# Kernel tuning notes

Hardware: AMD Instinct MI355X
Metric: run time of the kernel (lower is better)

The kernel has to match this reference:

```python
import jax, jax.numpy as jnp
import numpy as np
from jax import lax

NUM_HEADS = 8
DIM = 192
EPS = 1e-12  # torch F.normalize eps


def setup_inputs() -> dict:
    key = jax.random.key(0)
    k1, k2, k3, k4 = jax.random.split(key, 4)
    b, c, h, w = 8, DIM, 128, 128
    x = jax.random.normal(k1, (b, c, h, w), dtype=jnp.float32)
    # 1x1 qkv conv weight stored as [3c, c]; depthwise 3x3 weight [3c,1,3,3]; proj 1x1 [c,c]
    w_qkv = jax.random.normal(k2, (3 * c, c), dtype=jnp.float32) * (1.0 / np.sqrt(c))
    w_dw = jax.random.normal(k3, (3 * c, 1, 3, 3), dtype=jnp.float32) * (1.0 / 3.0)
    w_proj = jax.random.normal(k4, (c, c), dtype=jnp.float32) * (1.0 / np.sqrt(c))
    temperature = jnp.ones((NUM_HEADS, 1, 1), dtype=jnp.float32)
    return {"x": x, "w_qkv": w_qkv, "w_dw": w_dw, "w_proj": w_proj, "temperature": temperature}


def _l2_normalize(t):
    # matches torch.nn.functional.normalize(dim=-1, eps=1e-12)
    n = jnp.sqrt(jnp.sum(t * t, axis=-1, keepdims=True))
    return t / jnp.maximum(n, EPS)


def reference(x, w_qkv, w_dw, w_proj, temperature):
    b, c, h, w = x.shape
    heads = NUM_HEADS
    cd = c // heads  # per-head channel dim
    # 1x1 qkv conv (no bias) as einsum
    qkv = jnp.einsum('bchw,oc->bohw', x, w_qkv)  # [b, 3c, h, w]
    # depthwise 3x3 conv, groups = 3c
    qkv = lax.conv_general_dilated(
        qkv, w_dw, window_strides=(1, 1), padding='SAME',
        feature_group_count=3 * c,
        dimension_numbers=('NCHW', 'OIHW', 'NCHW'))
    q, k, v = jnp.split(qkv, 3, axis=1)  # each [b, c, h, w]
    hw = h * w
    q = q.reshape(b, heads, cd, hw)
    k = k.reshape(b, heads, cd, hw)
    v = v.reshape(b, heads, cd, hw)
    q = _l2_normalize(q)
    k = _l2_normalize(k)
    # channel-wise attention: [b, heads, cd, cd]
    attn = jnp.einsum('bhcn,bhdn->bhcd', q, k) * temperature[None]
    attn = jax.nn.softmax(attn, axis=-1)
    out = jnp.einsum('bhcd,bhdn->bhcn', attn, v)  # [b, heads, cd, hw]
    out = out.reshape(b, c, h, w)
    out = jnp.einsum('bchw,oc->bohw', out, w_proj)
    return out
```

## Files before the change

### kernel.cpp

```cpp
#include <hip/hip_runtime.h>

#define HW 16384
#define CC 192
#define C3 576
#define NB 8
#define NH 8

typedef __attribute__((ext_vector_type(8))) short bfrag;
typedef __attribute__((ext_vector_type(4))) float f32x4;
typedef __attribute__((ext_vector_type(4))) unsigned short us4;

#define MFMA16(a, b, c) __builtin_amdgcn_mfma_f32_16x16x32_bf16(a, b, c, 0, 0, 0)

typedef __attribute__((address_space(3))) unsigned int lds_u32;
typedef __attribute__((address_space(1))) unsigned int glb_u32;
__device__ __forceinline__ void gl_lds16(const void* g, void* l) {
  __builtin_amdgcn_global_load_lds((const glb_u32*)g, (lds_u32*)l, 16, 0, 0);
}

__device__ __forceinline__ unsigned short f2bf(float f) {
  unsigned int u = __float_as_uint(f);
  u += 0x7fffu + ((u >> 16) & 1u);
  return (unsigned short)(u >> 16);
}
__device__ __forceinline__ float bf2f(unsigned short s) {
  return __uint_as_float(((unsigned int)s) << 16);
}
__device__ __forceinline__ float bf2f_s(short s) {
  return __uint_as_float(((unsigned int)(unsigned short)s) << 16);
}

#define OFF_XT   0ull
#define SZ_XT    ((size_t)NB * HW * CC * 2)
#define OFF_WQ   (OFF_XT + SZ_XT)
#define SZ_WQ    ((size_t)C3 * CC * 2)
#define OFF_QKV  (OFF_WQ + SZ_WQ)
#define SZ_QKV   ((size_t)NB * C3 * HW * 2)
#define OFF_QKD  (OFF_QKV + SZ_QKV)
#define SZ_QKD   ((size_t)NB * 384 * HW * 2)
#define OFF_S    (OFF_QKD + SZ_QKD)
#define SZ_S     ((size_t)NB * NH * 32 * 32 * 4)
#define OFF_SSQ  (OFF_S + SZ_S)
#define SZ_SSQ   ((size_t)NB * 384 * 4)
#define OFF_M    (OFF_SSQ + SZ_SSQ)
#define SZ_M     ((size_t)NB * CC * CC * 2)

__global__ __launch_bounds__(256) void k_xt(const float* __restrict__ x,
                                            unsigned short* __restrict__ xt) {
  __shared__ unsigned short tile[64 * 72];
  const int pb = blockIdx.x * 64;
  const int cb = blockIdx.y * 64;
  const int b  = blockIdx.z;
  const int t  = threadIdx.x;
  {
    const int cl = t >> 2, pl = (t & 3) * 16;
    const float* src = x + ((size_t)b * CC + cb + cl) * HW + pb + pl;
    bfrag v0, v1;
#pragma unroll
    for (int q4 = 0; q4 < 2; ++q4) {
      float4 f = *reinterpret_cast<const float4*>(src + q4 * 4);
      v0[q4 * 4 + 0] = (short)f2bf(f.x); v0[q4 * 4 + 1] = (short)f2bf(f.y);
      v0[q4 * 4 + 2] = (short)f2bf(f.z); v0[q4 * 4 + 3] = (short)f2bf(f.w);
    }
#pragma unroll
    for (int q4 = 0; q4 < 2; ++q4) {
      float4 f = *reinterpret_cast<const float4*>(src + 8 + q4 * 4);
      v1[q4 * 4 + 0] = (short)f2bf(f.x); v1[q4 * 4 + 1] = (short)f2bf(f.y);
      v1[q4 * 4 + 2] = (short)f2bf(f.z); v1[q4 * 4 + 3] = (short)f2bf(f.w);
    }
    *reinterpret_cast<bfrag*>(&tile[cl * 72 + pl]) = v0;
    *reinterpret_cast<bfrag*>(&tile[cl * 72 + pl + 8]) = v1;
  }
  __syncthreads();
  {
    const int pl = t >> 2, cl = (t & 3) * 16;
    bfrag o0, o1;
#pragma unroll
    for (int e = 0; e < 8; ++e) o0[e] = (short)tile[(cl + e) * 72 + pl];
#pragma unroll
    for (int e = 0; e < 8; ++e) o1[e] = (short)tile[(cl + 8 + e) * 72 + pl];
    unsigned short* dst = xt + ((size_t)b * HW + pb + pl) * CC + cb + cl;
    *reinterpret_cast<bfrag*>(dst) = o0;
    *reinterpret_cast<bfrag*>(dst + 8) = o1;
  }
}

__global__ __launch_bounds__(256) void k_wpack(const float* __restrict__ w,
                                               unsigned short* __restrict__ wp) {
  const int g = blockIdx.x * 256 + threadIdx.x;
  if (g >= 216 * 64) return;
  const int frag = g >> 6, lane = g & 63;
  const int mb = frag / 24, r = frag % 24, s = r >> 2, i = r & 3;
  const int row = mb * 64 + i * 16 + (lane & 15);
  const int col = s * 32 + (lane >> 4) * 8;
  const float* src = w + (size_t)row * CC + col;
  float4 f0 = *reinterpret_cast<const float4*>(src);
  float4 f1 = *reinterpret_cast<const float4*>(src + 4);
  us4 o0, o1;
  o0[0] = f2bf(f0.x); o0[1] = f2bf(f0.y); o0[2] = f2bf(f0.z); o0[3] = f2bf(f0.w);
  o1[0] = f2bf(f1.x); o1[1] = f2bf(f1.y); o1[2] = f2bf(f1.z); o1[3] = f2bf(f1.w);
  *reinterpret_cast<us4*>(wp + (size_t)g * 8) = o0;
  *reinterpret_cast<us4*>(wp + (size_t)g * 8 + 4) = o1;
}

__global__ __launch_bounds__(256, 3) void k_gemm_qkv(const unsigned short* __restrict__ Wp,
                                                     const unsigned short* __restrict__ Xt,
                                                     unsigned short* __restrict__ Y) {
  __shared__ __attribute__((aligned(16))) char sB[49152];
  const int nb = blockIdx.x;
  const int b  = blockIdx.y;
  const int tid = threadIdx.x;
  const int wave = tid >> 6, lane = tid & 63;
  const int lrow = lane & 15, lk = (lane >> 4) * 8, lr4 = (lane >> 4) * 4;

  const char* Bc = (const char*)(Xt + ((size_t)b * HW + (size_t)nb * 128) * CC);
#pragma unroll
  for (int t = 0; t < 12; ++t) {
    const int L = wave * 12288 + t * 1024 + lane * 16;
    const int row = L / 384;
    const int rem = L - row * 384;
    gl_lds16(Bc + row * 384 + (rem ^ ((row & 7) << 4)), sB + wave * 12288 + t * 1024);
  }
  asm volatile("s_waitcnt vmcnt(0)" ::: "memory");
  __syncthreads();

  const int swz = (lrow & 7) << 4;
  const int base0 = (wave * 32 + lrow) * 384;
  const f32x4 z4 = {0.f, 0.f, 0.f, 0.f};

#pragma unroll 1
  for (int mb = 0; mb < 9; ++mb) {
    const unsigned short* Wb = Wp + (size_t)mb * 24 * 512;
    bfrag af[6][4];
#pragma unroll
    for (int s = 0; s < 6; ++s)
#pragma unroll
      for (int i = 0; i < 4; ++i)
        af[s][i] = *reinterpret_cast<const bfrag*>(Wb + ((s * 4 + i) * 64 + lane) * 8);

    f32x4 acc[4][2];
#pragma unroll
    for (int i = 0; i < 4; ++i) { acc[i][0] = z4; acc[i][1] = z4; }
#pragma unroll
    for (int s = 0; s < 6; ++s) {
      const int kbs = ((s * 32 + lk) * 2) ^ swz;
      bfrag b0 = *reinterpret_cast<const bfrag*>(sB + base0 + kbs);
      bfrag b1 = *reinterpret_cast<const bfrag*>(sB + base0 + 16 * 384 + kbs);
#pragma unroll
      for (int i = 0; i < 4; ++i) {
        acc[i][0] = MFMA16(b0, af[s][i], acc[i][0]);
        acc[i][1] = MFMA16(b1, af[s][i], acc[i][1]);
      }
    }
    unsigned short* Yb = Y + ((size_t)b * C3 + mb * 64) * HW + nb * 128 + wave * 32;
#pragma unroll
    for (int i = 0; i < 4; ++i) {
      unsigned short* rp = Yb + (size_t)(i * 16 + lrow) * HW;
#pragma unroll
      for (int j = 0; j < 2; ++j) {
        uint2 pk;
        pk.x = (unsigned int)f2bf(acc[i][j][0]) | ((unsigned int)f2bf(acc[i][j][1]) << 16);
        pk.y = (unsigned int)f2bf(acc[i][j][2]) | ((unsigned int)f2bf(acc[i][j][3]) << 16);
        *reinterpret_cast<uint2*>(rp + j * 16 + lr4) = pk;
      }
    }
  }
}

__global__ __launch_bounds__(256) void k_dwconv(const unsigned short* __restrict__ in,
                                                const float* __restrict__ wd,
                                                unsigned short* __restrict__ outb) {
  const int strip = blockIdx.x;
  const int ch = blockIdx.y;
  const int b = blockIdx.z;
  const int t = threadIdx.x;
  const unsigned short* ip = in + ((size_t)b * C3 + ch) * HW;
  const float* w = wd + ch * 9;
  const int p = strip * 2048 + t * 8;
  const int y = p >> 7, x0 = p & 127;
  float acc[8] = {0.f, 0.f, 0.f, 0.f, 0.f, 0.f, 0.f, 0.f};
#pragma unroll
  for (int dy = 0; dy < 3; ++dy) {
    int yy = y + dy - 1;
    if (yy < 0 || yy > 127) continue;
    const unsigned short* row = ip + yy * 128;
    bfrag v = *reinterpret_cast<const bfrag*>(row + x0);
    float c[8];
#pragma unroll
    for (int e = 0; e < 8; ++e) c[e] = bf2f_s(v[e]);
    float left  = (x0 > 0)   ? bf2f(row[x0 - 1]) : 0.f;
    float right = (x0 < 120) ? bf2f(row[x0 + 8]) : 0.f;
    float wl = w[dy * 3 + 0], wc = w[dy * 3 + 1], wr = w[dy * 3 + 2];
    acc[0] += wl * left + wc * c[0] + wr * c[1];
#pragma unroll
    for (int e = 1; e < 7; ++e) acc[e] += wl * c[e - 1] + wc * c[e] + wr * c[e + 1];
    acc[7] += wl * c[6] + wc * c[7] + wr * right;
  }
  unsigned short* op = outb + ((size_t)b * 384 + ch) * HW + p;
  bfrag o;
#pragma unroll
  for (int e = 0; e < 8; ++e) o[e] = (short)f2bf(acc[e]);
  *reinterpret_cast<bfrag*>(op) = o;
}

__global__ __launch_bounds__(256) void k_gram(const unsigned short* __restrict__ Qd,
                                              float* __restrict__ S,
                                              float* __restrict__ ssq) {
  const int chunk = blockIdx.x;
  const int h = blockIdx.y, b = blockIdx.z;
  const int tid = threadIdx.x, wave = tid >> 6, lane = tid & 63;
  const int lrow = lane & 15, lk8 = (lane >> 4) * 8;
  const unsigned short* qb = Qd + ((size_t)b * 384 + h * 24) * HW;
  const unsigned short* kb = qb + (size_t)192 * HW;
  const int p0 = chunk * 1024 + wave * 256;
  f32x4 acc[2][2];
  const f32x4 z4 = {0.f, 0.f, 0.f, 0.f};
#pragma unroll
  for (int i = 0; i < 2; ++i)
#pragma unroll
    for (int j = 0; j < 2; ++j) acc[i][j] = z4;
  float sq[2] = {0.f, 0.f}, sk[2] = {0.f, 0.f};
  for (int s = 0; s < 8; ++s) {
    const int pp = p0 + s * 32 + lk8;
    bfrag aq[2], bk[2];
#pragma unroll
    for (int i = 0; i < 2; ++i) {
      aq[i] = *reinterpret_cast<const bfrag*>(qb + (size_t)(i * 16 + lrow) * HW + pp);
      bk[i] = *reinterpret_cast<const bfrag*>(kb + (size_t)(i * 16 + lrow) * HW + pp);
    }
#pragma unroll
    for (int i = 0; i < 2; ++i) {
#pragma unroll
      for (int e = 0; e < 8; ++e) {
        float qv = bf2f_s(aq[i][e]); sq[i] += qv * qv;
        float kv = bf2f_s(bk[i][e]); sk[i] += kv * kv;
      }
    }
#pragma unroll
    for (int i = 0; i < 2; ++i)
#pragma unroll
      for (int j = 0; j < 2; ++j) acc[i][j] = MFMA16(aq[i], bk[j], acc[i][j]);
  }
  float* Sb = S + (size_t)(b * 8 + h) * 1024;
  const int lr4 = (lane >> 4) * 4;
#pragma unroll
  for (int i = 0; i < 2; ++i)
#pragma unroll
    for (int j = 0; j < 2; ++j)
#pragma unroll
      for (int r = 0; r < 4; ++r)
        atomicAdd(&Sb[(i * 16 + lr4 + r) * 32 + j * 16 + lrow], acc[i][j][r]);
#pragma unroll
  for (int i = 0; i < 2; ++i) {
    float v = sq[i];
    v += __shfl_xor(v, 16); v += __shfl_xor(v, 32);
    float wv = sk[i];
    wv += __shfl_xor(wv, 16); wv += __shfl_xor(wv, 32);
    const int c = i * 16 + lrow;
    if ((lane >> 4) == 0 && c < 24) {
      atomicAdd(&ssq[b * 384 + h * 24 + c], v);
      atomicAdd(&ssq[b * 384 + 192 + h * 24 + c], wv);
    }
  }
}

__global__ __launch_bounds__(256) void k_dwvt(const unsigned short* __restrict__ QKV,
                                              const float* __restrict__ wd,
                                              unsigned short* __restrict__ VTo) {
  __shared__ unsigned short tile[64 * 72];
  const int pb = blockIdx.x * 64, cb = blockIdx.y * 64, b = blockIdx.z;
  const int t = threadIdx.x;
  const int y = pb >> 7;
  const int xs = pb & 127;
  {
    const int cl = t >> 2, ps = (t & 3) * 16;
    const int gc = 384 + cb + cl;
    const unsigned short* ip = QKV + ((size_t)b * C3 + gc) * HW;
    const float* w = wd + gc * 9;
    const int x0 = xs + ps;
    float acc[16];
#pragma unroll
    for (int e = 0; e < 16; ++e) acc[e] = 0.f;
#pragma unroll
    for (int dy = 0; dy < 3; ++dy) {
      int yy = y + dy - 1;
      if (yy < 0 || yy > 127) continue;
      const unsigned short* row = ip + yy * 128;
      bfrag v0 = *reinterpret_cast<const bfrag*>(row + x0);
      bfrag v1 = *reinterpret_cast<const bfrag*>(row + x0 + 8);
      float c[16];
#pragma unroll
      for (int e = 0; e < 8; ++e) { c[e] = bf2f_s(v0[e]); c[8 + e] = bf2f_s(v1[e]); }
      float left  = (x0 > 0)   ? bf2f(row[x0 - 1])  : 0.f;
      float right = (x0 < 112) ? bf2f(row[x0 + 16]) : 0.f;
      float wl = w[dy * 3 + 0], wc = w[dy * 3 + 1], wr = w[dy * 3 + 2];
      acc[0] += wl * left + wc * c[0] + wr * c[1];
#pragma unroll
      for (int e = 1; e < 15; ++e) acc[e] += wl * c[e - 1] + wc * c[e] + wr * c[e + 1];
      acc[15] += wl * c[14] + wc * c[15] + wr * right;
    }
    bfrag o0, o1;
#pragma unroll
    for (int e = 0; e < 8; ++e) { o0[e] = (short)f2bf(acc[e]); o1[e] = (short)f2bf(acc[8 + e]); }
    *reinterpret_cast<bfrag*>(&tile[cl * 72 + ps]) = o0;
    *reinterpret_cast<bfrag*>(&tile[cl * 72 + ps + 8]) = o1;
  }
  __syncthreads();
  {
    const int pl = t >> 2, cs = (t & 3) * 16;
    bfrag o0, o1;
#pragma unroll
    for (int e = 0; e < 8; ++e) o0[e] = (short)tile[(cs + e) * 72 + pl];
#pragma unroll
    for (int e = 0; e < 8; ++e) o1[e] = (short)tile[(cs + 8 + e) * 72 + pl];
    unsigned short* dst = VTo + ((size_t)b * HW + pb + pl) * CC + cb + cs;
    *reinterpret_cast<bfrag*>(dst) = o0;
    *reinterpret_cast<bfrag*>(dst + 8) = o1;
  }
}

__global__ __launch_bounds__(64) void k_attn(const float* __restrict__ S,
                                             const float* __restrict__ ssq,
                                             const float* __restrict__ wproj,
                                             const float* __restrict__ temp,
                                             unsigned short* __restrict__ Mp) {
  const int h = blockIdx.x, b = blockIdx.y;
  __shared__ float A[24][25];
  __shared__ float nq[24], nk[24];
  const float* Sb = S + (size_t)(b * 8 + h) * 1024;
  const float* sq = ssq + b * 384 + h * 24;
  const float* sk = ssq + b * 384 + 192 + h * 24;
  const int t = threadIdx.x;
  if (t < 24) {
    nq[t] = fmaxf(sqrtf(sq[t]), 1e-12f);
    nk[t] = fmaxf(sqrtf(sk[t]), 1e-12f);
  }
  __syncthreads();
  if (t < 24) {
    const float tp = temp[h];
    float row[24];
    float mx = -1e30f;
#pragma unroll
    for (int d = 0; d < 24; ++d) {
      row[d] = Sb[t * 32 + d] / (nq[t] * nk[d]) * tp;
      mx = fmaxf(mx, row[d]);
    }
    float s = 0.f;
#pragma unroll
    for (int d = 0; d < 24; ++d) { row[d] = __expf(row[d] - mx); s += row[d]; }
    const float inv = 1.f / s;
#pragma unroll
    for (int d = 0; d < 24; ++d) A[t][d] = row[d] * inv;
  }
  __syncthreads();
  for (int idx = t; idx < 192 * 24; idx += 64) {
    const int o = idx / 24, dd = idx % 24;
    const float* wrow = wproj + o * 192 + h * 24;
    float a = 0.f;
#pragma unroll
    for (int cc = 0; cc < 24; ++cc) a += wrow[cc] * A[cc][dd];
    const int c = h * 24 + dd;
    const int mb = o >> 6, i = (o >> 4) & 3, lr = o & 15;
    const int s = c >> 5, hi = (c >> 3) & 3, e = c & 7;
    const int off = ((mb * 24 + s * 4 + i) * 64 + hi * 16 + lr) * 8 + e;
    Mp[(size_t)b * CC * CC + off] = f2bf(a);
  }
}

__global__ __launch_bounds__(256, 3) void k_gemm_out(const unsigned short* __restrict__ Mp,
                                                     const unsigned short* __restrict__ VT,
                                                     float* __restrict__ out) {
  __shared__ __attribute__((aligned(16))) char sB[49152];
  const int nb = blockIdx.x;
  const int b  = blockIdx.y;
  const int tid = threadIdx.x;
  const int wave = tid >> 6, lane = tid & 63;
  const int lrow = lane & 15, lk = (lane >> 4) * 8, lr4 = (lane >> 4) * 4;

  const char* Bc = (const char*)(VT + ((size_t)b * HW + (size_t)nb * 128) * CC);
#pragma unroll
  for (int t = 0; t < 12; ++t) {
    const int L = wave * 12288 + t * 1024 + lane * 16;
    const int row = L / 384;
    const int rem = L - row * 384;
    gl_lds16(Bc + row * 384 + (rem ^ ((row & 7) << 4)), sB + wave * 12288 + t * 1024);
  }
  asm volatile("s_waitcnt vmcnt(0)" ::: "memory");
  __syncthreads();

  const int swz = (lrow & 7) << 4;
  const int base0 = (wave * 32 + lrow) * 384;
  const f32x4 z4 = {0.f, 0.f, 0.f, 0.f};

#pragma unroll 1
  for (int mb = 0; mb < 3; ++mb) {
    const unsigned short* Mb = Mp + (size_t)b * CC * CC + (size_t)mb * 24 * 512;
    bfrag af[6][4];
#pragma unroll
    for (int s = 0; s < 6; ++s)
#pragma unroll
      for (int i = 0; i < 4; ++i)
        af[s][i] = *reinterpret_cast<const bfrag*>(Mb + ((s * 4 + i) * 64 + lane) * 8);

    f32x4 acc[4][2];
#pragma unroll
    for (int i = 0; i < 4; ++i) { acc[i][0] = z4; acc[i][1] = z4; }
#pragma unroll
    for (int s = 0; s < 6; ++s) {
      const int kbs = ((s * 32 + lk) * 2) ^ swz;
      bfrag b0 = *reinterpret_cast<const bfrag*>(sB + base0 + kbs);
      bfrag b1 = *reinterpret_cast<const bfrag*>(sB + base0 + 16 * 384 + kbs);
#pragma unroll
      for (int i = 0; i < 4; ++i) {
        acc[i][0] = MFMA16(b0, af[s][i], acc[i][0]);
        acc[i][1] = MFMA16(b1, af[s][i], acc[i][1]);
      }
    }
    float* Ob = out + ((size_t)b * CC + mb * 64) * HW + nb * 128 + wave * 32;
#pragma unroll
    for (int i = 0; i < 4; ++i) {
      float* rp = Ob + (size_t)(i * 16 + lrow) * HW;
#pragma unroll
      for (int j = 0; j < 2; ++j)
        *reinterpret_cast<f32x4*>(rp + j * 16 + lr4) = acc[i][j];
    }
  }
}

extern "C" void kernel_launch(void* const* d_in, const int* in_sizes, int n_in,
                              void* d_out, int out_size, void* d_ws, size_t ws_size,
                              hipStream_t stream) {
  const float* x      = (const float*)d_in[0];
  const float* w_qkv  = (const float*)d_in[1];
  const float* w_dw   = (const float*)d_in[2];
  const float* w_proj = (const float*)d_in[3];
  const float* temp   = (const float*)d_in[4];
  float* out = (float*)d_out;
  char* ws = (char*)d_ws;

  unsigned short* XT   = (unsigned short*)(ws + OFF_XT);
  unsigned short* VT   = (unsigned short*)(ws + OFF_XT);
  unsigned short* WP   = (unsigned short*)(ws + OFF_WQ);
  unsigned short* QKV  = (unsigned short*)(ws + OFF_QKV);
  unsigned short* QKD  = (unsigned short*)(ws + OFF_QKD);
  float* S   = (float*)(ws + OFF_S);
  float* SSQ = (float*)(ws + OFF_SSQ);
  unsigned short* MP  = (unsigned short*)(ws + OFF_M);

  hipMemsetAsync(ws + OFF_S, 0, SZ_S + SZ_SSQ, stream);
  k_wpack<<<54, 256, 0, stream>>>(w_qkv, WP);
  k_xt<<<dim3(HW / 64, CC / 64, NB), 256, 0, stream>>>(x, XT);
  k_gemm_qkv<<<dim3(HW / 128, NB), 256, 0, stream>>>(WP, XT, QKV);
  k_dwconv<<<dim3(8, 384, NB), 256, 0, stream>>>(QKV, w_dw, QKD);
  k_dwvt<<<dim3(HW / 64, 3, NB), 256, 0, stream>>>(QKV, w_dw, VT);
  k_gram<<<dim3(16, NH, NB), 256, 0, stream>>>(QKD, S, SSQ);
  k_attn<<<dim3(NH, NB), 64, 0, stream>>>(S, SSQ, w_proj, temp, MP);
  k_gemm_out<<<dim3(HW / 128, NB), 256, 0, stream>>>(MP, VT, out);
}
```

Baseline: 334.1 us.

## Store activations in MFMA fragment order and load B operands directly to registers

The producer kernels (k_xt, k_dwvt) now write the transposed bf16 activations in a layout that matches the MFMA fragment order per wave. The two GEMM kernels can then load their B operands straight into registers with coalesced 16-byte loads, with no LDS staging, swizzle or barrier. The GEMMs also switch to 512-thread blocks covering two 128-pixel tiles, and weight fragments are loaded per k-step instead of all up front. This removes LDS traffic and synchronisation in exchange for more register pressure and repeated global weight loads.

```diff
diff --git a/kernel.cpp b/kernel.cpp
--- a/kernel.cpp
+++ b/kernel.cpp
@@ -12,12 +12,6 @@
 
 #define MFMA16(a, b, c) __builtin_amdgcn_mfma_f32_16x16x32_bf16(a, b, c, 0, 0, 0)
 
-typedef __attribute__((address_space(3))) unsigned int lds_u32;
-typedef __attribute__((address_space(1))) unsigned int glb_u32;
-__device__ __forceinline__ void gl_lds16(const void* g, void* l) {
-  __builtin_amdgcn_global_load_lds((const glb_u32*)g, (lds_u32*)l, 16, 0, 0);
-}
-
 __device__ __forceinline__ unsigned short f2bf(float f) {
   unsigned int u = __float_as_uint(f);
   u += 0x7fffu + ((u >> 16) & 1u);
@@ -28,6 +22,10 @@
 }
 __device__ __forceinline__ float bf2f_s(short s) {
   return __uint_as_float(((unsigned int)(unsigned short)s) << 16);
+}
+
+__device__ __forceinline__ size_t faddr(int b, int tile, int w, int j, int s, int lane) {
+  return ((((((size_t)b * 128 + tile) * 4 + w) * 2 + j) * 6 + s) * 512 + (size_t)lane * 8);
 }
 
 #define OFF_XT   0ull
@@ -46,7 +44,7 @@
 #define SZ_M     ((size_t)NB * CC * CC * 2)
 
 __global__ __launch_bounds__(256) void k_xt(const float* __restrict__ x,
-                                            unsigned short* __restrict__ xt) {
+                                            unsigned short* __restrict__ xb) {
   __shared__ unsigned short tile[64 * 72];
   const int pb = blockIdx.x * 64;
   const int cb = blockIdx.y * 64;
@@ -79,9 +77,13 @@
     for (int e = 0; e < 8; ++e) o0[e] = (short)tile[(cl + e) * 72 + pl];
 #pragma unroll
     for (int e = 0; e < 8; ++e) o1[e] = (short)tile[(cl + 8 + e) * 72 + pl];
-    unsigned short* dst = xt + ((size_t)b * HW + pb + pl) * CC + cb + cl;
-    *reinterpret_cast<bfrag*>(dst) = o0;
-    *reinterpret_cast<bfrag*>(dst + 8) = o1;
+    const int P = pb + pl, ch0 = cb + cl;
+    const int ti = P >> 7, pit = P & 127;
+    const int w = pit >> 5, j = (pit >> 4) & 1, pxl = pit & 15;
+    const int s0 = ch0 >> 5, kh0 = (ch0 >> 3) & 3;
+    const int ch1 = ch0 + 8, s1 = ch1 >> 5, kh1 = (ch1 >> 3) & 3;
+    *reinterpret_cast<bfrag*>(xb + faddr(b, ti, w, j, s0, pxl + 16 * kh0)) = o0;
+    *reinterpret_cast<bfrag*>(xb + faddr(b, ti, w, j, s1, pxl + 16 * kh1)) = o1;
   }
 }
 
@@ -103,56 +105,43 @@
   *reinterpret_cast<us4*>(wp + (size_t)g * 8 + 4) = o1;
 }
 
-__global__ __launch_bounds__(256, 3) void k_gemm_qkv(const unsigned short* __restrict__ Wp,
-                                                     const unsigned short* __restrict__ Xt,
+__global__ __launch_bounds__(512, 4) void k_gemm_qkv(const unsigned short* __restrict__ Wp,
+                                                     const unsigned short* __restrict__ XB,
                                                      unsigned short* __restrict__ Y) {
-  __shared__ __attribute__((aligned(16))) char sB[49152];
   const int nb = blockIdx.x;
   const int b  = blockIdx.y;
   const int tid = threadIdx.x;
   const int wave = tid >> 6, lane = tid & 63;
-  const int lrow = lane & 15, lk = (lane >> 4) * 8, lr4 = (lane >> 4) * 4;
-
-  const char* Bc = (const char*)(Xt + ((size_t)b * HW + (size_t)nb * 128) * CC);
-#pragma unroll
-  for (int t = 0; t < 12; ++t) {
-    const int L = wave * 12288 + t * 1024 + lane * 16;
-    const int row = L / 384;
-    const int rem = L - row * 384;
-    gl_lds16(Bc + row * 384 + (rem ^ ((row & 7) << 4)), sB + wave * 12288 + t * 1024);
-  }
-  asm volatile("s_waitcnt vmcnt(0)" ::: "memory");
-  __syncthreads();
-
-  const int swz = (lrow & 7) << 4;
-  const int base0 = (wave * 32 + lrow) * 384;
+  const int lrow = lane & 15, lr4 = (lane >> 4) * 4;
+  const int tile = nb * 2 + (wave >> 2), w = wave & 3;
+
+  bfrag bq[2][6];
+#pragma unroll
+  for (int j = 0; j < 2; ++j)
+#pragma unroll
+    for (int s = 0; s < 6; ++s)
+      bq[j][s] = *reinterpret_cast<const bfrag*>(XB + faddr(b, tile, w, j, s, lane));
+
   const f32x4 z4 = {0.f, 0.f, 0.f, 0.f};
-
 #pragma unroll 1
   for (int mb = 0; mb < 9; ++mb) {
     const unsigned short* Wb = Wp + (size_t)mb * 24 * 512;
-    bfrag af[6][4];
-#pragma unroll
-    for (int s = 0; s < 6; ++s)
+    f32x4 acc[4][2];
+#pragma unroll
+    for (int i = 0; i < 4; ++i) { acc[i][0] = z4; acc[i][1] = z4; }
+#pragma unroll
+    for (int s = 0; s < 6; ++s) {
+      bfrag af[4];
 #pragma unroll
       for (int i = 0; i < 4; ++i)
-        af[s][i] = *reinterpret_cast<const bfrag*>(Wb + ((s * 4 + i) * 64 + lane) * 8);
-
-    f32x4 acc[4][2];
-#pragma unroll
-    for (int i = 0; i < 4; ++i) { acc[i][0] = z4; acc[i][1] = z4; }
-#pragma unroll
-    for (int s = 0; s < 6; ++s) {
-      const int kbs = ((s * 32 + lk) * 2) ^ swz;
-      bfrag b0 = *reinterpret_cast<const bfrag*>(sB + base0 + kbs);
-      bfrag b1 = *reinterpret_cast<const bfrag*>(sB + base0 + 16 * 384 + kbs);
+        af[i] = *reinterpret_cast<const bfrag*>(Wb + ((s * 4 + i) * 64 + lane) * 8);
 #pragma unroll
       for (int i = 0; i < 4; ++i) {
-        acc[i][0] = MFMA16(b0, af[s][i], acc[i][0]);
-        acc[i][1] = MFMA16(b1, af[s][i], acc[i][1]);
+        acc[i][0] = MFMA16(bq[0][s], af[i], acc[i][0]);
+        acc[i][1] = MFMA16(bq[1][s], af[i], acc[i][1]);
       }
     }
-    unsigned short* Yb = Y + ((size_t)b * C3 + mb * 64) * HW + nb * 128 + wave * 32;
+    unsigned short* Yb = Y + ((size_t)b * C3 + mb * 64) * HW + tile * 128 + w * 32;
 #pragma unroll
     for (int i = 0; i < 4; ++i) {
       unsigned short* rp = Yb + (size_t)(i * 16 + lrow) * HW;
@@ -313,9 +302,13 @@
     for (int e = 0; e < 8; ++e) o0[e] = (short)tile[(cs + e) * 72 + pl];
 #pragma unroll
     for (int e = 0; e < 8; ++e) o1[e] = (short)tile[(cs + 8 + e) * 72 + pl];
-    unsigned short* dst = VTo + ((size_t)b * HW + pb + pl) * CC + cb + cs;
-    *reinterpret_cast<bfrag*>(dst) = o0;
-    *reinterpret_cast<bfrag*>(dst + 8) = o1;
+    const int P = pb + pl, ch0 = cb + cs;
+    const int ti = P >> 7, pit = P & 127;
+    const int w = pit >> 5, j = (pit >> 4) & 1, pxl = pit & 15;
+    const int s0 = ch0 >> 5, kh0 = (ch0 >> 3) & 3;
+    const int ch1 = ch0 + 8, s1 = ch1 >> 5, kh1 = (ch1 >> 3) & 3;
+    *reinterpret_cast<bfrag*>(VTo + faddr(b, ti, w, j, s0, pxl + 16 * kh0)) = o0;
+    *reinterpret_cast<bfrag*>(VTo + faddr(b, ti, w, j, s1, pxl + 16 * kh1)) = o1;
   }
 }
 
@@ -367,56 +360,43 @@
   }
 }
 
-__global__ __launch_bounds__(256, 3) void k_gemm_out(const unsigned short* __restrict__ Mp,
-                                                     const unsigned short* __restrict__ VT,
+__global__ __launch_bounds__(512, 4) void k_gemm_out(const unsigned short* __restrict__ Mp,
+                                                     const unsigned short* __restrict__ VB,
                                                      float* __restrict__ out) {
-  __shared__ __attribute__((aligned(16))) char sB[49152];
   const int nb = blockIdx.x;
   const int b  = blockIdx.y;
   const int tid = threadIdx.x;
   const int wave = tid >> 6, lane = tid & 63;
-  const int lrow = lane & 15, lk = (lane >> 4) * 8, lr4 = (lane >> 4) * 4;
-
-  const char* Bc = (const char*)(VT + ((size_t)b * HW + (size_t)nb * 128) * CC);
-#pragma unroll
-  for (int t = 0; t < 12; ++t) {
-    const int L = wave * 12288 + t * 1024 + lane * 16;
-    const int row = L / 384;
-    const int rem = L - row * 384;
-    gl_lds16(Bc + row * 384 + (rem ^ ((row & 7) << 4)), sB + wave * 12288 + t * 1024);
-  }
-  asm volatile("s_waitcnt vmcnt(0)" ::: "memory");
-  __syncthreads();
-
-  const int swz = (lrow & 7) << 4;
-  const int base0 = (wave * 32 + lrow) * 384;
+  const int lrow = lane & 15, lr4 = (lane >> 4) * 4;
+  const int tile = nb * 2 + (wave >> 2), w = wave & 3;
+
+  bfrag bq[2][6];
+#pragma unroll
+  for (int j = 0; j < 2; ++j)
+#pragma unroll
+    for (int s = 0; s < 6; ++s)
+      bq[j][s] = *reinterpret_cast<const bfrag*>(VB + faddr(b, tile, w, j, s, lane));
+
   const f32x4 z4 = {0.f, 0.f, 0.f, 0.f};
-
 #pragma unroll 1
   for (int mb = 0; mb < 3; ++mb) {
     const unsigned short* Mb = Mp + (size_t)b * CC * CC + (size_t)mb * 24 * 512;
-    bfrag af[6][4];
-#pragma unroll
-    for (int s = 0; s < 6; ++s)
+    f32x4 acc[4][2];
+#pragma unroll
+    for (int i = 0; i < 4; ++i) { acc[i][0] = z4; acc[i][1] = z4; }
+#pragma unroll
+    for (int s = 0; s < 6; ++s) {
+      bfrag af[4];
 #pragma unroll
       for (int i = 0; i < 4; ++i)
-        af[s][i] = *reinterpret_cast<const bfrag*>(Mb + ((s * 4 + i) * 64 + lane) * 8);
-
-    f32x4 acc[4][2];
-#pragma unroll
-    for (int i = 0; i < 4; ++i) { acc[i][0] = z4; acc[i][1] = z4; }
-#pragma unroll
-    for (int s = 0; s < 6; ++s) {
-      const int kbs = ((s * 32 + lk) * 2) ^ swz;
-      bfrag b0 = *reinterpret_cast<const bfrag*>(sB + base0 + kbs);
-      bfrag b1 = *reinterpret_cast<const bfrag*>(sB + base0 + 16 * 384 + kbs);
+        af[i] = *reinterpret_cast<const bfrag*>(Mb + ((s * 4 + i) * 64 + lane) * 8);
 #pragma unroll
       for (int i = 0; i < 4; ++i) {
-        acc[i][0] = MFMA16(b0, af[s][i], acc[i][0]);
-        acc[i][1] = MFMA16(b1, af[s][i], acc[i][1]);
+        acc[i][0] = MFMA16(bq[0][s], af[i], acc[i][0]);
+        acc[i][1] = MFMA16(bq[1][s], af[i], acc[i][1]);
       }
     }
-    float* Ob = out + ((size_t)b * CC + mb * 64) * HW + nb * 128 + wave * 32;
+    float* Ob = out + ((size_t)b * CC + mb * 64) * HW + tile * 128 + w * 32;
 #pragma unroll
     for (int i = 0; i < 4; ++i) {
       float* rp = Ob + (size_t)(i * 16 + lrow) * HW;
@@ -438,8 +418,8 @@
   float* out = (float*)d_out;
   char* ws = (char*)d_ws;
 
-  unsigned short* XT   = (unsigned short*)(ws + OFF_XT);
-  unsigned short* VT   = (unsigned short*)(ws + OFF_XT);
+  unsigned short* XB   = (unsigned short*)(ws + OFF_XT);
+  unsigned short* VB   = (unsigned short*)(ws + OFF_XT);
   unsigned short* WP   = (unsigned short*)(ws + OFF_WQ);
   unsigned short* QKV  = (unsigned short*)(ws + OFF_QKV);
   unsigned short* QKD  = (unsigned short*)(ws + OFF_QKD);
@@ -449,11 +429,11 @@
 
   hipMemsetAsync(ws + OFF_S, 0, SZ_S + SZ_SSQ, stream);
   k_wpack<<<54, 256, 0, stream>>>(w_qkv, WP);
-  k_xt<<<dim3(HW / 64, CC / 64, NB), 256, 0, stream>>>(x, XT);
-  k_gemm_qkv<<<dim3(HW / 128, NB), 256, 0, stream>>>(WP, XT, QKV);
+  k_xt<<<dim3(HW / 64, CC / 64, NB), 256, 0, stream>>>(x, XB);
+  k_gemm_qkv<<<dim3(64, NB), 512, 0, stream>>>(WP, XB, QKV);
   k_dwconv<<<dim3(8, 384, NB), 256, 0, stream>>>(QKV, w_dw, QKD);
-  k_dwvt<<<dim3(HW / 64, 3, NB), 256, 0, stream>>>(QKV, w_dw, VT);
+  k_dwvt<<<dim3(HW / 64, 3, NB), 256, 0, stream>>>(QKV, w_dw, VB);
   k_gram<<<dim3(16, NH, NB), 256, 0, stream>>>(QKD, S, SSQ);
   k_attn<<<dim3(NH, NB), 64, 0, stream>>>(S, SSQ, w_proj, temp, MP);
-  k_gemm_out<<<dim3(HW / 128, NB), 256, 0, stream>>>(MP, VT, out);
-}
+  k_gemm_out<<<dim3(64, NB), 512, 0, stream>>>(MP, VB, out);
+}
```

Measured after the change: 322.1 us. 1.04x faster.
